# Kernel optimization log

Measured on AMD Instinct MI355X. Metric: run time of the kernel, lower is better.

Reference implementation:

```python
import jax, jax.numpy as jnp
import numpy as np

D_MODEL = 1024
N_HEADS = 16
HEAD_DIM = D_MODEL // N_HEADS
B, T = 4, 2048


def setup_inputs() -> dict:
    key = jax.random.key(0)
    ks = jax.random.split(key, 9)
    s = 1.0 / np.sqrt(D_MODEL)
    x = jax.random.normal(ks[0], (B, T, D_MODEL), dtype=jnp.float32)
    # causal mask: 1 = attend, 0 = blocked (masked_fill(mask == 0, -inf))
    mask = jnp.tril(jnp.ones((T, T), dtype=jnp.int32))[None, None, :, :]
    Wq = jax.random.uniform(ks[1], (D_MODEL, D_MODEL), jnp.float32, -s, s)
    bq = jax.random.uniform(ks[2], (D_MODEL,), jnp.float32, -s, s)
    Wk = jax.random.uniform(ks[3], (D_MODEL, D_MODEL), jnp.float32, -s, s)
    bk = jax.random.uniform(ks[4], (D_MODEL,), jnp.float32, -s, s)
    Wv = jax.random.uniform(ks[5], (D_MODEL, D_MODEL), jnp.float32, -s, s)
    bv = jax.random.uniform(ks[6], (D_MODEL,), jnp.float32, -s, s)
    Wo = jax.random.uniform(ks[7], (D_MODEL, D_MODEL), jnp.float32, -s, s)
    bo = jax.random.uniform(ks[8], (D_MODEL,), jnp.float32, -s, s)
    return {"x": x, "mask": mask, "Wq": Wq, "bq": bq, "Wk": Wk, "bk": bk,
            "Wv": Wv, "bv": bv, "Wo": Wo, "bo": bo}


def reference(x, mask, Wq, bq, Wk, bk, Wv, bv, Wo, bo):
    # nn.Linear: y = x @ W.T + b; here W stored as [in, out] so y = x @ W + b
    Bsz, Tlen, C = x.shape
    scale = jnp.sqrt(jnp.float32(HEAD_DIM))

    def split_heads(t):  # [B,T,C] -> [B,H,T,hd]
        return t.reshape(Bsz, Tlen, N_HEADS, HEAD_DIM).transpose(0, 2, 1, 3)

    Q = split_heads(x @ Wq + bq)
    K = split_heads(x @ Wk + bk)
    V = split_heads(x @ Wv + bv)

    scores = jnp.einsum("bhqd,bhkd->bhqk", Q, K) / scale
    scores = jnp.where(mask == 0, jnp.float32(-jnp.inf), scores)
    weights = jax.nn.softmax(scores, axis=-1)  # dropout is identity (eval/p=0)
    out = jnp.einsum("bhqk,bhkd->bhqd", weights, V)
    out = out.transpose(0, 2, 1, 3).reshape(Bsz, Tlen, C)
    return out @ Wo + bo
```

## Files before the change

kernel.cpp:

```cpp
#include <hip/hip_runtime.h>
#include <cstdint>
#include <cstddef>

#define B_SZ 4
#define T_SZ 2048
#define NH 16
#define HD 64
#define CD 1024
#define MROWS (B_SZ*T_SZ)
#define NEG_BIG (-1e30f)
#define Q_SCALE 0.180336880f

typedef __bf16 bf16x8 __attribute__((ext_vector_type(8)));
typedef __bf16 bf16x4 __attribute__((ext_vector_type(4)));
typedef short s16x4 __attribute__((ext_vector_type(4)));
typedef float f32x4 __attribute__((ext_vector_type(4)));

typedef __attribute__((address_space(3))) void* as3p;
typedef const __attribute__((address_space(1))) void* as1p;

__device__ __forceinline__ void glds16(const void* g, void* l) {
  __builtin_amdgcn_global_load_lds((as1p)g, (as3p)l, 16, 0, 0);
}

__global__ __launch_bounds__(256) void detect_dtype(const uint32_t* __restrict__ x,
                                                    int* __restrict__ flag) {
  __shared__ int cnt[256];
  const int t = threadIdx.x;
  int c = 0;
  for (int i = 0; i < 4; i++) {
    uint32_t w = x[t * 4 + i];
    uint32_t e = (w >> 7) & 0xFF;
    c += (e >= 100 && e <= 140) ? 1 : 0;
  }
  cnt[t] = c;
  __syncthreads();
  for (int s = 128; s > 0; s >>= 1) {
    if (t < s) cnt[t] += cnt[t + s];
    __syncthreads();
  }
  if (t == 0) flag[0] = (cnt[0] > 700) ? 1 : 0;
}

__device__ __forceinline__ bf16x8 cvt8(const void* src, int isbf, size_t i8) {
  bf16x8 o;
  if (isbf) {
    o = ((const bf16x8*)src)[i8];
  } else {
    const float4* s = (const float4*)((const float*)src + i8 * 8);
    float4 a = s[0], b = s[1];
    o[0] = (__bf16)a.x; o[1] = (__bf16)a.y; o[2] = (__bf16)a.z; o[3] = (__bf16)a.w;
    o[4] = (__bf16)b.x; o[5] = (__bf16)b.y; o[6] = (__bf16)b.z; o[7] = (__bf16)b.w;
  }
  return o;
}

__global__ __launch_bounds__(256) void conv_in(const void* __restrict__ src,
                                               const int* __restrict__ flag,
                                               __bf16* __restrict__ dst, int n8) {
  int i = blockIdx.x * 256 + threadIdx.x;
  if (i >= n8) return;
  ((bf16x8*)dst)[i] = cvt8(src, flag[0], i);
}

struct Ptr4 { const void* s[4]; __bf16* d[4]; };

__global__ __launch_bounds__(256) void conv_b4(Ptr4 p, const int* __restrict__ flag) {
  int i = threadIdx.x;
  if (i >= CD / 8) return;
  int which = blockIdx.x;
  ((bf16x8*)p.d[which])[i] = cvt8(p.s[which], flag[0], i);
}

__global__ __launch_bounds__(256) void transpose_conv4(Ptr4 p,
                                                       const int* __restrict__ flag) {
  __shared__ __align__(16) __bf16 tile[64 * 72];
  const void* W = p.s[blockIdx.z];
  __bf16* WT = p.d[blockIdx.z];
  const int t = threadIdx.x;
  const int r0 = blockIdx.y * 64, c0 = blockIdx.x * 64;
  const int rr = t >> 3, c8 = (t & 7) * 8;
  const int isbf = flag[0];
  for (int pp = 0; pp < 2; pp++) {
    int r = pp * 32 + rr;
    *(bf16x8*)(tile + r * 72 + c8) =
        cvt8(W, isbf, ((size_t)(r0 + r) * CD + c0 + c8) / 8);
  }
  __syncthreads();
  for (int pp = 0; pp < 2; pp++) {
    int cc = pp * 32 + rr;
    bf16x8 o;
    for (int j = 0; j < 8; j++) o[j] = tile[(c8 + j) * 72 + cc];
    *(bf16x8*)(WT + (size_t)(c0 + cc) * CD + r0 + c8) = o;
  }
}

__global__ __launch_bounds__(256) void gemm_qkv(
    const __bf16* __restrict__ A, const __bf16* __restrict__ BT,
    const __bf16* __restrict__ bias,
    __bf16* __restrict__ Qb, __bf16* __restrict__ Kb, __bf16* __restrict__ Vt) {
  __shared__ __align__(16) __bf16 As[128 * 64];
  __shared__ __align__(16) __bf16 Bs[128 * 64];
  const int tid = threadIdx.x;
  const int w = tid >> 6, lane = tid & 63;
  const int l15 = lane & 15, quad = lane >> 4;
  const int wm = w & 1, wn = w >> 1;
  const int bm = blockIdx.y, bn = blockIdx.x;
  const bool swapped = (bn < 16);

  f32x4 acc[4][4];
  for (int i = 0; i < 4; i++)
    for (int j = 0; j < 4; j++) acc[i][j] = (f32x4)0.f;

  const int srow = lane >> 3, scol = (lane & 7) * 8;
  const int scolsw = scol ^ (srow * 8);
  const __bf16* Abase = A + (size_t)(bm * 128) * CD;
  const __bf16* Bbase = BT + (size_t)(bn * 128) * CD;

  const int swz = (l15 & 7) * 8;
  for (int k0 = 0; k0 < CD; k0 += 64) {
    __syncthreads();
    for (int p = 0; p < 4; p++) {
      int seg = p * 4 + w;
      int row = seg * 8 + srow;
      glds16(Abase + (size_t)row * CD + k0 + scolsw, (char*)As + seg * 1024);
      glds16(Bbase + (size_t)row * CD + k0 + scolsw, (char*)Bs + seg * 1024);
    }
    __syncthreads();
    for (int kc = 0; kc < 2; kc++) {
      const int koff = (kc * 32 + quad * 8) ^ swz;
      bf16x8 af[4], bfr[4];
      for (int mt = 0; mt < 4; mt++)
        af[mt] = *(const bf16x8*)(As + (wm * 64 + mt * 16 + l15) * 64 + koff);
      for (int nt = 0; nt < 4; nt++)
        bfr[nt] = *(const bf16x8*)(Bs + (wn * 64 + nt * 16 + l15) * 64 + koff);
      if (swapped) {
        for (int mt = 0; mt < 4; mt++)
          for (int nt = 0; nt < 4; nt++)
            acc[mt][nt] = __builtin_amdgcn_mfma_f32_16x16x32_bf16(
                bfr[nt], af[mt], acc[mt][nt], 0, 0, 0);
      } else {
        for (int mt = 0; mt < 4; mt++)
          for (int nt = 0; nt < 4; nt++)
            acc[mt][nt] = __builtin_amdgcn_mfma_f32_16x16x32_bf16(
                af[mt], bfr[nt], acc[mt][nt], 0, 0, 0);
      }
    }
  }

  if (swapped) {
    const int hq = (bn & 7) * 2 + wn;
    const int bq_ = bm >> 4;
    const int tokb = (bm & 15) * 128 + wm * 64;
    __bf16* dst = (bn < 8) ? Qb : Kb;
    const float sc = (bn < 8) ? Q_SCALE : 1.f;
    for (int nt = 0; nt < 4; nt++) {
      const int d0 = nt * 16 + quad * 4;
      bf16x4 bv4 = *(const bf16x4*)(bias + bn * 128 + wn * 64 + d0);
      for (int mt = 0; mt < 4; mt++) {
        int tok = tokb + mt * 16 + l15;
        bf16x4 o;
        for (int r = 0; r < 4; r++)
          o[r] = (__bf16)((acc[mt][nt][r] + (float)bv4[r]) * sc);
        *(bf16x4*)(dst + ((size_t)(bq_ * NH + hq) * T_SZ + tok) * HD + d0) = o;
      }
    }
  } else {
    for (int nt = 0; nt < 4; nt++) {
      int col = bn * 128 + wn * 64 + nt * 16 + l15;
      int c = col & 1023, h = c >> 6, d = c & 63;
      float bv = (float)bias[col];
      for (int mt = 0; mt < 4; mt++) {
        int row0 = bm * 128 + wm * 64 + mt * 16 + quad * 4;
        int b = row0 >> 11, tok0 = row0 & 2047;
        bf16x4 o;
        for (int r = 0; r < 4; r++) o[r] = (__bf16)(acc[mt][nt][r] + bv);
        *(bf16x4*)(Vt + ((size_t)((b << 4) + h) * HD + d) * T_SZ + tok0) = o;
      }
    }
  }
}

__global__ __launch_bounds__(256) void gemm_out(
    const __bf16* __restrict__ A, const __bf16* __restrict__ BT,
    const __bf16* __restrict__ bias, void* __restrict__ Out,
    const int* __restrict__ flag) {
  __shared__ __align__(16) __bf16 As[128 * 64];
  __shared__ __align__(16) __bf16 Bs[128 * 64];
  const int tid = threadIdx.x;
  const int w = tid >> 6, lane = tid & 63;
  const int l15 = lane & 15, quad = lane >> 4;
  const int wm = w & 1, wn = w >> 1;
  const int bm = blockIdx.y, bn = blockIdx.x;

  f32x4 acc[4][4];
  for (int i = 0; i < 4; i++)
    for (int j = 0; j < 4; j++) acc[i][j] = (f32x4)0.f;

  const int srow = lane >> 3, scol = (lane & 7) * 8;
  const int scolsw = scol ^ (srow * 8);
  const __bf16* Abase = A + (size_t)(bm * 128) * CD;
  const __bf16* Bbase = BT + (size_t)(bn * 128) * CD;

  const int swz = (l15 & 7) * 8;
  for (int k0 = 0; k0 < CD; k0 += 64) {
    __syncthreads();
    for (int p = 0; p < 4; p++) {
      int seg = p * 4 + w;
      int row = seg * 8 + srow;
      glds16(Abase + (size_t)row * CD + k0 + scolsw, (char*)As + seg * 1024);
      glds16(Bbase + (size_t)row * CD + k0 + scolsw, (char*)Bs + seg * 1024);
    }
    __syncthreads();
    for (int kc = 0; kc < 2; kc++) {
      const int koff = (kc * 32 + quad * 8) ^ swz;
      bf16x8 af[4], bfr[4];
      for (int mt = 0; mt < 4; mt++)
        af[mt] = *(const bf16x8*)(As + (wm * 64 + mt * 16 + l15) * 64 + koff);
      for (int nt = 0; nt < 4; nt++)
        bfr[nt] = *(const bf16x8*)(Bs + (wn * 64 + nt * 16 + l15) * 64 + koff);
      for (int mt = 0; mt < 4; mt++)
        for (int nt = 0; nt < 4; nt++)
          acc[mt][nt] = __builtin_amdgcn_mfma_f32_16x16x32_bf16(
              bfr[nt], af[mt], acc[mt][nt], 0, 0, 0);
    }
  }

  const int isbf = flag[0];
  for (int nt = 0; nt < 4; nt++) {
    const int colb = bn * 128 + wn * 64 + nt * 16 + quad * 4;
    bf16x4 bv4 = *(const bf16x4*)(bias + colb);
    for (int mt = 0; mt < 4; mt++) {
      int row = bm * 128 + wm * 64 + mt * 16 + l15;
      if (isbf) {
        bf16x4 o;
        for (int r = 0; r < 4; r++)
          o[r] = (__bf16)(acc[mt][nt][r] + (float)bv4[r]);
        *(bf16x4*)((__bf16*)Out + (size_t)row * CD + colb) = o;
      } else {
        f32x4 o;
        for (int r = 0; r < 4; r++) o[r] = acc[mt][nt][r] + (float)bv4[r];
        *(f32x4*)((float*)Out + (size_t)row * CD + colb) = o;
      }
    }
  }
}

__global__ __launch_bounds__(512, 4) void attn(
    const __bf16* __restrict__ Q, const __bf16* __restrict__ K,
    const __bf16* __restrict__ Vt, __bf16* __restrict__ Y) {
  __shared__ __align__(16) __bf16 Ks[2][64 * 64];
  __shared__ __align__(16) __bf16 Vs[2][64 * 76];

  const int tid = threadIdx.x, w = tid >> 6, lane = tid & 63;
  const int l15 = lane & 15, quad = lane >> 4;
  const int lid = blockIdx.x + 8 * blockIdx.y;
  const int bh = lid & 63;
  const int pairi = lid >> 6;

  const __bf16* Qbh = Q + (size_t)bh * T_SZ * HD;
  const __bf16* Kbh = K + (size_t)bh * T_SZ * HD;
  const __bf16* Vbh = Vt + (size_t)bh * HD * T_SZ;

  const int srow = tid >> 3;
  const int scol = (tid & 7) * 8;
  const int kwcol = scol ^ ((srow & 7) * 8);
  const int b = bh >> 4, h = bh & 15;

  bf16x4 ones;
  for (int r = 0; r < 4; r++) ones[r] = (__bf16)1.0f;

  for (int ph = 0; ph < 2; ph++) {
    const int tq = ph ? (15 - pairi) : pairi;
    const int q0 = tq * 128;
    const int niter = 2 * tq + 2;
    const int qw = q0 + w * 16;

    __syncthreads();
    *(bf16x8*)(Ks[0] + srow * 64 + kwcol) =
        *(const bf16x8*)(Kbh + (size_t)srow * HD + scol);
    {
      bf16x8 v0 = *(const bf16x8*)(Vbh + (size_t)srow * T_SZ + scol);
      *(bf16x4*)(Vs[0] + srow * 76 + scol)     = ((bf16x4*)&v0)[0];
      *(bf16x4*)(Vs[0] + srow * 76 + scol + 4) = ((bf16x4*)&v0)[1];
    }

    bf16x8 aq[2];
    for (int kc = 0; kc < 2; kc++)
      aq[kc] = *(const bf16x8*)(
          Qbh + (size_t)(qw + l15) * HD + kc * 32 + quad * 8);

    f32x4 acco[4];
    for (int dt = 0; dt < 4; dt++) acco[dt] = (f32x4)0.f;
    f32x4 accl = (f32x4)0.f;
    float m_ = NEG_BIG;

    for (int it = 0; it < niter; it++) {
      const int cur = it & 1;
      const int kv0 = it * 64;
      __syncthreads();

      bf16x8 kn, vn;
      const bool havenext = (it + 1 < niter);
      if (havenext) {
        int kv1 = kv0 + 64;
        kn = *(const bf16x8*)(Kbh + (size_t)(kv1 + srow) * HD + scol);
        vn = *(const bf16x8*)(Vbh + (size_t)srow * T_SZ + kv1 + scol);
      }

      if (kv0 <= qw + 15) {
        const __bf16* Ksc = Ks[cur];
        const __bf16* Vsc = Vs[cur];

        f32x4 accs[4];
        for (int nt = 0; nt < 4; nt++) accs[nt] = (f32x4)0.f;
        const int swz = (l15 & 7) * 8;
        for (int kc = 0; kc < 2; kc++)
          for (int nt = 0; nt < 4; nt++) {
            bf16x8 ak = *(const bf16x8*)(
                Ksc + (nt * 16 + l15) * 64 + ((kc * 32 + quad * 8) ^ swz));
            accs[nt] = __builtin_amdgcn_mfma_f32_16x16x32_bf16(
                ak, aq[kc], accs[nt], 0, 0, 0);
          }

        if (kv0 + 63 > qw) {
          int qg = qw + l15;
          for (int nt = 0; nt < 4; nt++) {
            int kg0 = kv0 + nt * 16 + quad * 4;
            for (int r = 0; r < 4; r++)
              if (kg0 + r > qg) accs[nt][r] = NEG_BIG;
          }
        }

        float t0 = fmaxf(fmaxf(accs[0][0], accs[0][1]), accs[0][2]);
        float t1 = fmaxf(fmaxf(accs[0][3], accs[1][0]), accs[1][1]);
        float t2 = fmaxf(fmaxf(accs[1][2], accs[1][3]), accs[2][0]);
        float t3 = fmaxf(fmaxf(accs[2][1], accs[2][2]), accs[2][3]);
        float t4 = fmaxf(fmaxf(accs[3][0], accs[3][1]), accs[3][2]);
        float t5 = fmaxf(fmaxf(t0, t1), t2);
        float t6 = fmaxf(fmaxf(t3, t4), accs[3][3]);
        float mloc = fmaxf(t5, t6);
        mloc = fmaxf(mloc, __shfl_xor(mloc, 16));
        mloc = fmaxf(mloc, __shfl_xor(mloc, 32));

        if (!__all(mloc <= m_)) {
          float mnew = fmaxf(m_, mloc);
          float alpha = __builtin_amdgcn_exp2f(m_ - mnew);
          m_ = mnew;
          accl[0] *= alpha;
          for (int dt = 0; dt < 4; dt++)
            for (int r = 0; r < 4; r++) acco[dt][r] *= alpha;
        }

        bf16x4 pf[4];
        for (int nt = 0; nt < 4; nt++)
          for (int r = 0; r < 4; r++)
            pf[nt][r] = (__bf16)__builtin_amdgcn_exp2f(accs[nt][r] - m_);

        for (int nt = 0; nt < 4; nt++) {
          accl = __builtin_amdgcn_mfma_f32_16x16x16bf16_1k(
              *(const s16x4*)&ones, *(const s16x4*)&pf[nt], accl, 0, 0, 0);
          for (int dt = 0; dt < 4; dt++) {
            bf16x4 av = *(const bf16x4*)(Vsc + (dt * 16 + l15) * 76 + nt * 16 + quad * 4);
            acco[dt] = __builtin_amdgcn_mfma_f32_16x16x16bf16_1k(
                *(const s16x4*)&av, *(const s16x4*)&pf[nt], acco[dt], 0, 0, 0);
          }
        }
      }

      if (havenext) {
        int nb = cur ^ 1;
        *(bf16x8*)(Ks[nb] + srow * 64 + kwcol) = kn;
        *(bf16x4*)(Vs[nb] + srow * 76 + scol)     = ((bf16x4*)&vn)[0];
        *(bf16x4*)(Vs[nb] + srow * 76 + scol + 4) = ((bf16x4*)&vn)[1];
      }
    }

    {
      float rcp = 1.f / accl[0];
      int qg = qw + l15;
      size_t base = ((size_t)(b * T_SZ + qg)) * CD + h * HD + quad * 4;
      for (int dt = 0; dt < 4; dt++) {
        bf16x4 o;
        for (int r = 0; r < 4; r++) o[r] = (__bf16)(acco[dt][r] * rcp);
        *(bf16x4*)(Y + base + dt * 16) = o;
      }
    }
  }
}

extern "C" void kernel_launch(void* const* d_in, const int* in_sizes, int n_in,
                              void* d_out, int out_size, void* d_ws, size_t ws_size,
                              hipStream_t stream) {
  (void)in_sizes; (void)n_in; (void)out_size; (void)ws_size;
  const void* x  = d_in[0];
  const void* Wq = d_in[2];
  const void* bq = d_in[3];
  const void* Wk = d_in[4];
  const void* bk = d_in[5];
  const void* Wv = d_in[6];
  const void* bv = d_in[7];
  const void* Wo = d_in[8];
  const void* bo = d_in[9];

  char* ws = (char*)d_ws;
  const size_t MB = 1024 * 1024;
  __bf16* WqkvT = (__bf16*)(ws + 0 * MB);
  __bf16* WoT   = (__bf16*)(ws + 6 * MB);
  __bf16* bqkvc = (__bf16*)(ws + 8 * MB);
  __bf16* boc   = (__bf16*)(ws + 8 * MB + 8192);
  int*    flag  = (int*)   (ws + 8 * MB + 65536);
  __bf16* xc    = (__bf16*)(ws + 9 * MB);
  __bf16* Qb    = (__bf16*)(ws + 25 * MB);
  __bf16* Kb    = (__bf16*)(ws + 41 * MB);
  __bf16* Vt_g  = (__bf16*)(ws + 57 * MB);
  __bf16* Yb    = xc;

  dim3 tb(256);
  detect_dtype<<<1, tb, 0, stream>>>((const uint32_t*)x, flag);

  conv_in<<<4096, tb, 0, stream>>>(x, flag, xc, MROWS * CD / 8);
  Ptr4 pb = {{bq, bk, bv, bo}, {bqkvc, bqkvc + CD, bqkvc + 2 * CD, boc}};
  conv_b4<<<4, tb, 0, stream>>>(pb, flag);
  Ptr4 pw = {{Wq, Wk, Wv, Wo},
             {WqkvT, WqkvT + (size_t)CD * CD, WqkvT + 2 * (size_t)CD * CD, WoT}};
  transpose_conv4<<<dim3(16, 16, 4), tb, 0, stream>>>(pw, flag);

  gemm_qkv<<<dim3(24, MROWS / 128), tb, 0, stream>>>(xc, WqkvT, bqkvc, Qb, Kb, Vt_g);

  attn<<<dim3(8, B_SZ * NH), dim3(512), 0, stream>>>(Qb, Kb, Vt_g, Yb);

  gemm_out<<<dim3(CD / 128, MROWS / 128), tb, 0, stream>>>(Yb, WoT, boc, d_out, flag);
}
```

Baseline: 275.7 us.

## Load K via direct global-to-LDS and read V straight from global memory

K tiles are now staged with global_load_lds (async direct-to-LDS), with the XOR swizzle moved from the LDS write address to the global source column. The V shared-memory buffer is removed entirely and each wave reads its V fragments directly from global (transposed V) into registers before the softmax. This cuts the register round trip and the LDS write traffic for staging. In exchange V is re-read from global/L2 by every wave, using narrow 8-byte loads instead of a shared tile, and there is no explicit wait on the direct LDS load before the next barrier.

```diff
diff --git a/kernel.cpp b/kernel.cpp
--- a/kernel.cpp
+++ b/kernel.cpp
@@ -250,7 +250,6 @@
     const __bf16* __restrict__ Q, const __bf16* __restrict__ K,
     const __bf16* __restrict__ Vt, __bf16* __restrict__ Y) {
   __shared__ __align__(16) __bf16 Ks[2][64 * 64];
-  __shared__ __align__(16) __bf16 Vs[2][64 * 76];
 
   const int tid = threadIdx.x, w = tid >> 6, lane = tid & 63;
   const int l15 = lane & 15, quad = lane >> 4;
@@ -264,7 +263,7 @@
 
   const int srow = tid >> 3;
   const int scol = (tid & 7) * 8;
-  const int kwcol = scol ^ ((srow & 7) * 8);
+  const int ksrc = scol ^ ((srow & 7) * 8);
   const int b = bh >> 4, h = bh & 15;
 
   bf16x4 ones;
@@ -277,13 +276,7 @@
     const int qw = q0 + w * 16;
 
     __syncthreads();
-    *(bf16x8*)(Ks[0] + srow * 64 + kwcol) =
-        *(const bf16x8*)(Kbh + (size_t)srow * HD + scol);
-    {
-      bf16x8 v0 = *(const bf16x8*)(Vbh + (size_t)srow * T_SZ + scol);
-      *(bf16x4*)(Vs[0] + srow * 76 + scol)     = ((bf16x4*)&v0)[0];
-      *(bf16x4*)(Vs[0] + srow * 76 + scol + 4) = ((bf16x4*)&v0)[1];
-    }
+    glds16(Kbh + (size_t)srow * HD + ksrc, (char*)Ks[0] + w * 1024);
 
     bf16x8 aq[2];
     for (int kc = 0; kc < 2; kc++)
@@ -300,17 +293,12 @@
       const int kv0 = it * 64;
       __syncthreads();
 
-      bf16x8 kn, vn;
-      const bool havenext = (it + 1 < niter);
-      if (havenext) {
-        int kv1 = kv0 + 64;
-        kn = *(const bf16x8*)(Kbh + (size_t)(kv1 + srow) * HD + scol);
-        vn = *(const bf16x8*)(Vbh + (size_t)srow * T_SZ + kv1 + scol);
-      }
+      if (it + 1 < niter)
+        glds16(Kbh + (size_t)(kv0 + 64 + srow) * HD + ksrc,
+               (char*)Ks[cur ^ 1] + w * 1024);
 
       if (kv0 <= qw + 15) {
         const __bf16* Ksc = Ks[cur];
-        const __bf16* Vsc = Vs[cur];
 
         f32x4 accs[4];
         for (int nt = 0; nt < 4; nt++) accs[nt] = (f32x4)0.f;
@@ -323,6 +311,14 @@
                 ak, aq[kc], accs[nt], 0, 0, 0);
           }
 
+        bf16x4 av[4][4];
+#pragma unroll
+        for (int nt = 0; nt < 4; nt++)
+#pragma unroll
+          for (int dt = 0; dt < 4; dt++)
+            av[nt][dt] = *(const bf16x4*)(
+                Vbh + (size_t)(dt * 16 + l15) * T_SZ + kv0 + nt * 16 + quad * 4);
+
         if (kv0 + 63 > qw) {
           int qg = qw + l15;
           for (int nt = 0; nt < 4; nt++) {
@@ -357,22 +353,16 @@
           for (int r = 0; r < 4; r++)
             pf[nt][r] = (__bf16)__builtin_amdgcn_exp2f(accs[nt][r] - m_);
 
+#pragma unroll
         for (int nt = 0; nt < 4; nt++) {
           accl = __builtin_amdgcn_mfma_f32_16x16x16bf16_1k(
               *(const s16x4*)&ones, *(const s16x4*)&pf[nt], accl, 0, 0, 0);
-          for (int dt = 0; dt < 4; dt++) {
-            bf16x4 av = *(const bf16x4*)(Vsc + (dt * 16 + l15) * 76 + nt * 16 + quad * 4);
+#pragma unroll
+          for (int dt = 0; dt < 4; dt++)
             acco[dt] = __builtin_amdgcn_mfma_f32_16x16x16bf16_1k(
-                *(const s16x4*)&av, *(const s16x4*)&pf[nt], acco[dt], 0, 0, 0);
-          }
+                *(const s16x4*)&av[nt][dt], *(const s16x4*)&pf[nt],
+                acco[dt], 0, 0, 0);
         }
-      }
-
-      if (havenext) {
-        int nb = cur ^ 1;
-        *(bf16x8*)(Ks[nb] + srow * 64 + kwcol) = kn;
-        *(bf16x4*)(Vs[nb] + srow * 76 + scol)     = ((bf16x4*)&vn)[0];
-        *(bf16x4*)(Vs[nb] + srow * 76 + scol + 4) = ((bf16x4*)&vn)[1];
       }
     }
 
```

Result: slower. 471.5 us (+71.0%).

## Double attention KV tile to 128 and load K directly to LDS

Applied to the files above, without the earlier changes.

Doubles the key/value tile from 64 to 128 per iteration, which halves the number of loop iterations and barriers, and widens the score and PV MFMA loops to match. K tiles are now loaded with global_load_lds into LDS, using an XOR-swizzled source address in place of the swizzled LDS write. LDS use roughly doubles, which may reduce occupancy, and causal masking now wastes more work on diagonal tiles.

```diff
diff --git a/kernel.cpp b/kernel.cpp
--- a/kernel.cpp
+++ b/kernel.cpp
@@ -249,8 +249,8 @@
 __global__ __launch_bounds__(512, 4) void attn(
     const __bf16* __restrict__ Q, const __bf16* __restrict__ K,
     const __bf16* __restrict__ Vt, __bf16* __restrict__ Y) {
-  __shared__ __align__(16) __bf16 Ks[2][64 * 64];
-  __shared__ __align__(16) __bf16 Vs[2][64 * 76];
+  __shared__ __align__(16) __bf16 Ks[2][128 * 64];
+  __shared__ __align__(16) __bf16 Vs[2][64 * 140];
 
   const int tid = threadIdx.x, w = tid >> 6, lane = tid & 63;
   const int l15 = lane & 15, quad = lane >> 4;
@@ -264,7 +264,7 @@
 
   const int srow = tid >> 3;
   const int scol = (tid & 7) * 8;
-  const int kwcol = scol ^ ((srow & 7) * 8);
+  const int ksrc = scol ^ ((srow & 7) * 8);
   const int b = bh >> 4, h = bh & 15;
 
   bf16x4 ones;
@@ -273,16 +273,20 @@
   for (int ph = 0; ph < 2; ph++) {
     const int tq = ph ? (15 - pairi) : pairi;
     const int q0 = tq * 128;
-    const int niter = 2 * tq + 2;
+    const int niter = tq + 1;
     const int qw = q0 + w * 16;
 
     __syncthreads();
-    *(bf16x8*)(Ks[0] + srow * 64 + kwcol) =
-        *(const bf16x8*)(Kbh + (size_t)srow * HD + scol);
+    glds16(Kbh + (size_t)srow * HD + ksrc, (char*)Ks[0] + w * 1024);
+    glds16(Kbh + (size_t)(64 + srow) * HD + ksrc,
+           (char*)Ks[0] + 8192 + w * 1024);
     {
-      bf16x8 v0 = *(const bf16x8*)(Vbh + (size_t)srow * T_SZ + scol);
-      *(bf16x4*)(Vs[0] + srow * 76 + scol)     = ((bf16x4*)&v0)[0];
-      *(bf16x4*)(Vs[0] + srow * 76 + scol + 4) = ((bf16x4*)&v0)[1];
+      bf16x8 va = *(const bf16x8*)(Vbh + (size_t)srow * T_SZ + scol);
+      bf16x8 vb = *(const bf16x8*)(Vbh + (size_t)srow * T_SZ + 64 + scol);
+      *(bf16x4*)(Vs[0] + srow * 140 + scol)          = ((bf16x4*)&va)[0];
+      *(bf16x4*)(Vs[0] + srow * 140 + scol + 4)      = ((bf16x4*)&va)[1];
+      *(bf16x4*)(Vs[0] + srow * 140 + 64 + scol)     = ((bf16x4*)&vb)[0];
+      *(bf16x4*)(Vs[0] + srow * 140 + 64 + scol + 4) = ((bf16x4*)&vb)[1];
     }
 
     bf16x8 aq[2];
@@ -297,49 +301,52 @@
 
     for (int it = 0; it < niter; it++) {
       const int cur = it & 1;
-      const int kv0 = it * 64;
+      const int kv0 = it * 128;
       __syncthreads();
 
-      bf16x8 kn, vn;
+      bf16x8 vna, vnb;
       const bool havenext = (it + 1 < niter);
       if (havenext) {
-        int kv1 = kv0 + 64;
-        kn = *(const bf16x8*)(Kbh + (size_t)(kv1 + srow) * HD + scol);
-        vn = *(const bf16x8*)(Vbh + (size_t)srow * T_SZ + kv1 + scol);
+        int kv1 = kv0 + 128;
+        glds16(Kbh + (size_t)(kv1 + srow) * HD + ksrc,
+               (char*)Ks[cur ^ 1] + w * 1024);
+        glds16(Kbh + (size_t)(kv1 + 64 + srow) * HD + ksrc,
+               (char*)Ks[cur ^ 1] + 8192 + w * 1024);
+        vna = *(const bf16x8*)(Vbh + (size_t)srow * T_SZ + kv1 + scol);
+        vnb = *(const bf16x8*)(Vbh + (size_t)srow * T_SZ + kv1 + 64 + scol);
       }
 
       if (kv0 <= qw + 15) {
         const __bf16* Ksc = Ks[cur];
         const __bf16* Vsc = Vs[cur];
 
-        f32x4 accs[4];
-        for (int nt = 0; nt < 4; nt++) accs[nt] = (f32x4)0.f;
+        f32x4 accs[8];
+        for (int nt = 0; nt < 8; nt++) accs[nt] = (f32x4)0.f;
         const int swz = (l15 & 7) * 8;
         for (int kc = 0; kc < 2; kc++)
-          for (int nt = 0; nt < 4; nt++) {
+          for (int nt = 0; nt < 8; nt++) {
             bf16x8 ak = *(const bf16x8*)(
                 Ksc + (nt * 16 + l15) * 64 + ((kc * 32 + quad * 8) ^ swz));
             accs[nt] = __builtin_amdgcn_mfma_f32_16x16x32_bf16(
                 ak, aq[kc], accs[nt], 0, 0, 0);
           }
 
-        if (kv0 + 63 > qw) {
+        if (kv0 + 127 > qw) {
           int qg = qw + l15;
-          for (int nt = 0; nt < 4; nt++) {
+          for (int nt = 0; nt < 8; nt++) {
             int kg0 = kv0 + nt * 16 + quad * 4;
             for (int r = 0; r < 4; r++)
               if (kg0 + r > qg) accs[nt][r] = NEG_BIG;
           }
         }
 
-        float t0 = fmaxf(fmaxf(accs[0][0], accs[0][1]), accs[0][2]);
-        float t1 = fmaxf(fmaxf(accs[0][3], accs[1][0]), accs[1][1]);
-        float t2 = fmaxf(fmaxf(accs[1][2], accs[1][3]), accs[2][0]);
-        float t3 = fmaxf(fmaxf(accs[2][1], accs[2][2]), accs[2][3]);
-        float t4 = fmaxf(fmaxf(accs[3][0], accs[3][1]), accs[3][2]);
-        float t5 = fmaxf(fmaxf(t0, t1), t2);
-        float t6 = fmaxf(fmaxf(t3, t4), accs[3][3]);
-        float mloc = fmaxf(t5, t6);
+        float tm[8];
+        for (int nt = 0; nt < 8; nt++)
+          tm[nt] = fmaxf(fmaxf(accs[nt][0], accs[nt][1]),
+                         fmaxf(accs[nt][2], accs[nt][3]));
+        float u0 = fmaxf(fmaxf(tm[0], tm[1]), fmaxf(tm[2], tm[3]));
+        float u1 = fmaxf(fmaxf(tm[4], tm[5]), fmaxf(tm[6], tm[7]));
+        float mloc = fmaxf(u0, u1);
         mloc = fmaxf(mloc, __shfl_xor(mloc, 16));
         mloc = fmaxf(mloc, __shfl_xor(mloc, 32));
 
@@ -352,16 +359,19 @@
             for (int r = 0; r < 4; r++) acco[dt][r] *= alpha;
         }
 
-        bf16x4 pf[4];
-        for (int nt = 0; nt < 4; nt++)
+        bf16x4 pf[8];
+        for (int nt = 0; nt < 8; nt++)
           for (int r = 0; r < 4; r++)
             pf[nt][r] = (__bf16)__builtin_amdgcn_exp2f(accs[nt][r] - m_);
 
-        for (int nt = 0; nt < 4; nt++) {
+#pragma unroll
+        for (int nt = 0; nt < 8; nt++) {
           accl = __builtin_amdgcn_mfma_f32_16x16x16bf16_1k(
               *(const s16x4*)&ones, *(const s16x4*)&pf[nt], accl, 0, 0, 0);
+#pragma unroll
           for (int dt = 0; dt < 4; dt++) {
-            bf16x4 av = *(const bf16x4*)(Vsc + (dt * 16 + l15) * 76 + nt * 16 + quad * 4);
+            bf16x4 av = *(const bf16x4*)(
+                Vsc + (dt * 16 + l15) * 140 + nt * 16 + quad * 4);
             acco[dt] = __builtin_amdgcn_mfma_f32_16x16x16bf16_1k(
                 *(const s16x4*)&av, *(const s16x4*)&pf[nt], acco[dt], 0, 0, 0);
           }
@@ -370,9 +380,10 @@
 
       if (havenext) {
         int nb = cur ^ 1;
-        *(bf16x8*)(Ks[nb] + srow * 64 + kwcol) = kn;
-        *(bf16x4*)(Vs[nb] + srow * 76 + scol)     = ((bf16x4*)&vn)[0];
-        *(bf16x4*)(Vs[nb] + srow * 76 + scol + 4) = ((bf16x4*)&vn)[1];
+        *(bf16x4*)(Vs[nb] + srow * 140 + scol)          = ((bf16x4*)&vna)[0];
+        *(bf16x4*)(Vs[nb] + srow * 140 + scol + 4)      = ((bf16x4*)&vna)[1];
+        *(bf16x4*)(Vs[nb] + srow * 140 + 64 + scol)     = ((bf16x4*)&vnb)[0];
+        *(bf16x4*)(Vs[nb] + srow * 140 + 64 + scol + 4) = ((bf16x4*)&vnb)[1];
       }
     }
 
```

After: 276.8 us. About the same (+0.4%).
